# Kernel tuning notes

Measured on AMD Instinct MI355X. Metric: run time of the kernel, lower is better.

## Reference

```python
import jax, jax.numpy as jnp
import numpy as np

B, H, T, D = 2, 8, 2048, 64
STATE = H * D  # 512

def setup_inputs() -> dict:
    key = jax.random.key(0)
    kq, kk, kv, kw, kl = jax.random.split(key, 5)
    q = jax.random.normal(kq, (B * H, T, D), jnp.float32)
    k = jax.random.normal(kk, (B * H, T, D), jnp.float32)
    v = jax.random.normal(kv, (B * H, T, D), jnp.float32)
    # causal position mask: True = masked (future positions)
    position_mask = jnp.triu(jnp.ones((T, T), dtype=bool), 1)
    # per-batch source lengths in [T//2, T]; True = padding (masked)
    lengths = jax.random.randint(kl, (B,), T // 2, T + 1)
    src_length_mask = jnp.arange(T)[None, :] >= lengths[:, None]
    W_merge = jax.random.normal(kw, (STATE, STATE), jnp.float32) / np.sqrt(STATE)
    return {"q": q, "k": k, "v": v, "position_mask": position_mask,
            "src_length_mask": src_length_mask, "W_merge": W_merge}

def reference(q, k, v, position_mask, src_length_mask, W_merge):
    bb, n_dest, d = q.shape              # bb = B*H
    n_batch = src_length_mask.shape[0]
    n_heads = bb // n_batch
    scale = 1.0 / np.sqrt(d)
    # [bb, T_dest, T_src] full score matrix (as in the torch bmm)
    logits = jnp.einsum('btd,bsd->bts', q, k) * scale
    logits = logits.reshape(n_batch, n_heads, n_dest, -1)
    logits = jnp.where(position_mask[None, None], -jnp.inf, logits)
    logits = jnp.where(src_length_mask[:, None, None, :], -jnp.inf, logits)
    scores = jax.nn.softmax(logits, axis=-1).reshape(bb, n_dest, -1)
    # dropout p=0 (eval) -> identity
    out = jnp.einsum('bts,bsd->btd', scores, v)
    out = out.reshape(n_batch, n_heads, n_dest, d).transpose(0, 2, 1, 3)
    out = out.reshape(n_batch, n_dest, n_heads * d)
    return out @ W_merge.T  # bias-free Linear merge
```

## Files before the change

kernel.cpp:

```cpp
#include <hip/hip_runtime.h>

#define TT 2048
#define DD 64
#define NSTATE 512

typedef __attribute__((ext_vector_type(8))) short short8;
typedef __attribute__((ext_vector_type(4))) short short4v;
typedef __attribute__((ext_vector_type(4))) float f4;

__device__ __forceinline__ short f2bf(float x) {
  union { float f; unsigned u; } c; c.f = x;
  unsigned r = (c.u + 0x7FFFu + ((c.u >> 16) & 1u)) >> 16;
  return (short)r;
}

__device__ __forceinline__ bool mask_at(const void* p, bool u8, int idx) {
  return u8 ? (((const unsigned char*)p)[idx] != 0)
            : (((const int*)p)[idx] != 0);
}

__device__ __forceinline__ void gld16(const void* g, void* l) {
  __builtin_amdgcn_global_load_lds(
      (const __attribute__((address_space(1))) void*)g,
      (__attribute__((address_space(3))) void*)l, 16, 0, 0);
}

__global__ __launch_bounds__(256)
void prep_kernel(const float* __restrict__ k, const float* __restrict__ v,
                 const float* __restrict__ W, const void* __restrict__ posmask,
                 const void* __restrict__ srcmask,
                 unsigned short* __restrict__ Wb, unsigned short* __restrict__ Kimg,
                 unsigned short* __restrict__ VTimg, int* __restrict__ lenbuf) {
  const int bidx = blockIdx.x;
  const int tid = threadIdx.x;
  if (bidx < 512) {
    const int bh = bidx >> 5, tile = bidx & 31;
    const float* kp = k + (bh * TT + tile * 64) * DD;
    unsigned short* dst = Kimg + (bh * 32 + tile) * 4096;
#pragma unroll
    for (int t2 = 0; t2 < 2; ++t2) {
      int j = tid + t2 * 256;
      int c8 = j >> 6, r6 = j & 63;
      int kb = c8 >> 1, cc = c8 & 1, qd = r6 >> 4, klo = r6 & 15;
      int key = kb * 16 + klo, dg = cc * 4 + qd;
      f4 a0 = *(const f4*)(kp + key * DD + dg * 8);
      f4 a1 = *(const f4*)(kp + key * DD + dg * 8 + 4);
      short8 o;
      o[0]=f2bf(a0[0]); o[1]=f2bf(a0[1]); o[2]=f2bf(a0[2]); o[3]=f2bf(a0[3]);
      o[4]=f2bf(a1[0]); o[5]=f2bf(a1[1]); o[6]=f2bf(a1[2]); o[7]=f2bf(a1[3]);
      *(short8*)(dst + j * 8) = o;
    }
    __shared__ float Vt[64][65];
    const float* vp = v + (bh * TT + tile * 64) * DD;
    {
      int key = tid >> 2, c0 = (tid & 3) * 16;
#pragma unroll
      for (int i = 0; i < 4; ++i) {
        f4 x = *(const f4*)(vp + key * DD + c0 + i * 4);
        Vt[key][c0 + i * 4 + 0] = x[0];
        Vt[key][c0 + i * 4 + 1] = x[1];
        Vt[key][c0 + i * 4 + 2] = x[2];
        Vt[key][c0 + i * 4 + 3] = x[3];
      }
    }
    __syncthreads();
    unsigned short* vd = VTimg + (bh * 32 + tile) * 4096;
#pragma unroll
    for (int t2 = 0; t2 < 2; ++t2) {
      int j = tid + t2 * 256;
      int fs = j >> 5;
      int db = fs >> 2, sb = fs & 3;
      int jj = j & 31;
      short8 o;
#pragma unroll
      for (int ii = 0; ii < 8; ++ii) {
        int l = jj * 2 + (ii >> 2), r = ii & 3;
        int s = sb * 16 + (l >> 4) * 4 + r;
        int d = db * 16 + (l & 15);
        o[ii] = f2bf(Vt[s][d]);
      }
      *(short8*)(vd + j * 8) = o;
    }
  } else if (bidx < 768) {
    int i = ((bidx - 512) * 256 + tid) * 4;
    f4 x = *(const f4*)(W + i);
    short4v o;
    o[0]=f2bf(x[0]); o[1]=f2bf(x[1]); o[2]=f2bf(x[2]); o[3]=f2bf(x[3]);
    *(short4v*)(Wb + i) = o;
  } else {
    const int wv = tid >> 6, lane = tid & 63;
    if (wv < 2) {
      const bool u8 = (((const unsigned char*)posmask)[1] != 0);
      int pos = 1024 + lane * 16;
      bool m1 = mask_at(srcmask, u8, wv * TT + pos);
      unsigned long long bal = __ballot(m1);
      int cur = bal ? (1024 + (__ffsll((unsigned long long)bal) - 1) * 16) : 2048;
      int prev = cur - 16;
      bool m2 = false;
      if (lane < 16) {
        int pos2 = prev + 1 + lane;
        m2 = (pos2 < TT) ? mask_at(srcmask, u8, wv * TT + pos2) : true;
      }
      unsigned long long bal2 = __ballot(m2);
      int len = prev + 1 + (__ffsll((unsigned long long)bal2) - 1);
      if (lane == 0) lenbuf[wv] = len;
    }
  }
}

__global__ __launch_bounds__(512, 4)
void attn_kernel(const float* __restrict__ q, const unsigned short* __restrict__ Kimg,
                 const unsigned short* __restrict__ VTimg,
                 const int* __restrict__ lenbuf, unsigned short* __restrict__ merged) {
  const int i = blockIdx.x;
  const int bh = ((i & 7) << 1) | ((i >> 3) & 1);
  const int tr = i >> 4;
  const int tile = (tr < 16) ? tr : 47 - tr;
  const int b = bh >> 3, h = bh & 7;
  const int tid = threadIdx.x;
  const int w = tid >> 6, lane = tid & 63;
  const int g = w >> 2, wl = w & 3;
  const int lane_lo = lane & 15, quad = lane >> 4;
  const int q0 = tile * 64 + wl * 16;
  const int len = lenbuf[b];
  const int n_st = min(tile + 1, (len + 63) >> 6);
  const int trips = (n_st + 1) >> 1;

  __shared__ __attribute__((aligned(16))) unsigned short Klds[2][2][4096];
  __shared__ __attribute__((aligned(16))) unsigned short Vlds[2][2][4096];

  short8 qf[2];
  {
    const float* qrow = q + ((bh * TT) + q0 + lane_lo) * DD;
#pragma unroll
    for (int c = 0; c < 2; ++c) {
      int d0 = c * 32 + quad * 8;
      f4 a0 = *(const f4*)(qrow + d0);
      f4 a1 = *(const f4*)(qrow + d0 + 4);
      short8 t;
      t[0]=f2bf(a0[0]*0.125f); t[1]=f2bf(a0[1]*0.125f);
      t[2]=f2bf(a0[2]*0.125f); t[3]=f2bf(a0[3]*0.125f);
      t[4]=f2bf(a1[0]*0.125f); t[5]=f2bf(a1[1]*0.125f);
      t[6]=f2bf(a1[2]*0.125f); t[7]=f2bf(a1[3]*0.125f);
      qf[c] = t;
    }
  }

  float l_lane = 0.f;
  f4 O[4];
#pragma unroll
  for (int d = 0; d < 4; ++d) O[d] = (f4){0.f, 0.f, 0.f, 0.f};

  const char* kbase = (const char*)Kimg + (size_t)bh * 262144;
  const char* vbase = (const char*)VTimg + (size_t)bh * 262144;

  auto stage = [&](int st, int bufi) {
    const char* ks = kbase + st * 8192 + wl * 2048 + lane * 16;
    char* kl = (char*)&Klds[g][bufi][0] + wl * 2048 + lane * 16;
    gld16(ks, kl); gld16(ks + 1024, kl + 1024);
    const char* vs = vbase + st * 8192 + wl * 2048 + lane * 16;
    char* vl = (char*)&Vlds[g][bufi][0] + wl * 2048 + lane * 16;
    gld16(vs, vl); gld16(vs + 1024, vl + 1024);
  };

  if (g < n_st) stage(g, 0);
  __syncthreads();

  for (int it = 0; it < trips; ++it) {
    const int st = 2 * it + g;
    const int bufc = it & 1;
    const int st_next = st + 2;
    if (st_next < n_st) stage(st_next, bufc ^ 1);
    if (st < n_st) {
      const unsigned short* Kl = &Klds[g][bufc][0];
      const unsigned short* Vl = &Vlds[g][bufc][0];
      const int s0 = st * 64;

      f4 ST[4];
      __builtin_amdgcn_s_setprio(1);
#pragma unroll
      for (int sb = 0; sb < 4; ++sb) {
        f4 acc = (f4){0.f, 0.f, 0.f, 0.f};
#pragma unroll
        for (int c = 0; c < 2; ++c) {
          short8 kf = *(const short8*)&Kl[((sb * 2 + c) * 64 + lane) * 8];
          acc = __builtin_amdgcn_mfma_f32_16x16x32_bf16(kf, qf[c], acc, 0, 0, 0);
        }
        ST[sb] = acc;
      }
      __builtin_amdgcn_s_setprio(0);

      const bool edge = (st == tile) || (s0 + 64 > len);
      const int tq = q0 + lane_lo;
      short4v pf[4];
#pragma unroll
      for (int sb = 0; sb < 4; ++sb)
#pragma unroll
        for (int r = 0; r < 4; ++r) {
          float p = __expf(ST[sb][r]);
          if (edge) {
            int s = s0 + sb * 16 + quad * 4 + r;
            if (s > tq || s >= len) p = 0.f;
          }
          l_lane += p;
          pf[sb][r] = f2bf(p);
        }

      __builtin_amdgcn_s_setprio(1);
#pragma unroll
      for (int db = 0; db < 4; ++db) {
        f4 acc = O[db];
#pragma unroll
        for (int sb = 0; sb < 4; ++sb) {
          short4v vf = *(const short4v*)&Vl[(db * 4 + sb) * 256 + lane * 4];
          acc = __builtin_amdgcn_mfma_f32_16x16x16bf16_1k(pf[sb], vf, acc, 0, 0, 0);
        }
        O[db] = acc;
      }
      __builtin_amdgcn_s_setprio(0);
    }
    __syncthreads();
  }

  l_lane += __shfl_xor(l_lane, 16);
  l_lane += __shfl_xor(l_lane, 32);

  float* Ored = (float*)&Klds[1][0][0];
  float* lred = (float*)&Vlds[1][0][0];
  if (g == 1) {
    float* po = Ored + (wl * 64 + lane) * 16;
#pragma unroll
    for (int db = 0; db < 4; ++db) *(f4*)(po + db * 4) = O[db];
    lred[wl * 64 + lane] = l_lane;
  }
  __syncthreads();
  if (g == 0) {
    const float* po = Ored + (wl * 64 + lane) * 16;
#pragma unroll
    for (int db = 0; db < 4; ++db) {
      f4 o1 = *(const f4*)(po + db * 4);
      O[db][0] += o1[0]; O[db][1] += o1[1];
      O[db][2] += o1[2]; O[db][3] += o1[3];
    }
    l_lane += lred[wl * 64 + lane];
    float inv = 1.0f / l_lane;
    float invr[4];
#pragma unroll
    for (int r = 0; r < 4; ++r) invr[r] = __shfl(inv, quad * 4 + r);
#pragma unroll
    for (int db = 0; db < 4; ++db)
#pragma unroll
      for (int r = 0; r < 4; ++r) {
        int t = q0 + quad * 4 + r;
        merged[((b * TT) + t) * NSTATE + h * DD + db * 16 + lane_lo] =
            (unsigned short)f2bf(O[db][r] * invr[r]);
      }
  }
}

__global__ __launch_bounds__(512)
void merge_kernel(const unsigned short* __restrict__ A,
                  const unsigned short* __restrict__ Wb,
                  float* __restrict__ out) {
  __shared__ __attribute__((aligned(16))) unsigned short Wl[64 * 512];
  const int tid = threadIdx.x;
  const int n0 = blockIdx.x * 64, m0 = blockIdx.y * 128;
  {
    int row = tid >> 3, cb = (tid & 7) * 8;
    const unsigned short* src = Wb + (n0 + row) * NSTATE;
#pragma unroll
    for (int j = 0; j < 8; ++j) {
      int c = cb + j;
      int phys = c ^ (row & 7);
      *(short8*)&Wl[row * 512 + phys * 8] = *(const short8*)(src + c * 8);
    }
  }
  __syncthreads();

  const int w = tid >> 6, lane = tid & 63;
  const int lo16 = lane & 15, quad = lane >> 4;
  const int m = m0 + w * 16;
  f4 acc[4];
#pragma unroll
  for (int nf = 0; nf < 4; ++nf) acc[nf] = (f4){0.f, 0.f, 0.f, 0.f};
  const unsigned short* arow = A + (m + lo16) * NSTATE + quad * 8;
#pragma unroll 4
  for (int k0 = 0; k0 < NSTATE; k0 += 32) {
    short8 af = *(const short8*)(arow + k0);
#pragma unroll
    for (int nf = 0; nf < 4; ++nf) {
      int n = nf * 16 + lo16;
      int phys = ((k0 >> 3) + quad) ^ (n & 7);
      short8 bf = *(const short8*)&Wl[n * 512 + phys * 8];
      acc[nf] = __builtin_amdgcn_mfma_f32_16x16x32_bf16(af, bf, acc[nf], 0, 0, 0);
    }
  }
#pragma unroll
  for (int nf = 0; nf < 4; ++nf)
#pragma unroll
    for (int r = 0; r < 4; ++r)
      out[(m + quad * 4 + r) * NSTATE + n0 + nf * 16 + lo16] = acc[nf][r];
}

extern "C" void kernel_launch(void* const* d_in, const int* in_sizes, int n_in,
                              void* d_out, int out_size, void* d_ws, size_t ws_size,
                              hipStream_t stream) {
  (void)in_sizes; (void)n_in; (void)out_size; (void)ws_size;
  const float* q = (const float*)d_in[0];
  const float* k = (const float*)d_in[1];
  const float* v = (const float*)d_in[2];
  const void* posm = d_in[3];
  const void* srcm = d_in[4];
  const float* W = (const float*)d_in[5];
  float* out = (float*)d_out;

  unsigned short* merged = (unsigned short*)d_ws;
  unsigned short* Wb     = merged + 2097152;
  unsigned short* Kimg   = Wb + 262144;
  unsigned short* VTimg  = Kimg + 2097152;
  int* lenbuf = (int*)(VTimg + 2097152);

  prep_kernel<<<dim3(769), dim3(256), 0, stream>>>(k, v, W, posm, srcm,
                                                   Wb, Kimg, VTimg, lenbuf);
  attn_kernel<<<dim3(512), dim3(512), 0, stream>>>(q, Kimg, VTimg, lenbuf, merged);
  merge_kernel<<<dim3(8, 32), dim3(512), 0, stream>>>(merged, Wb, out);
}
```

Measured before the change: 122.2 us.

## Use hardware bf16 pack conversion and partial vmcnt waits in attention loop

Replaces the software round-to-nearest bf16 conversion with the packed v_cvt_pk_bf16_f32 instruction across the prep, attention and output paths. In the attention loop, the full __syncthreads is swapped for explicit s_waitcnt vmcnt(4)/vmcnt(0) plus a raw s_barrier with sched_barrier fences. Only the current stage's async LDS loads are waited on, so the prefetch of the next stage stays in flight. This cuts conversion ALU work and lets loads overlap compute, but relies on hand-counted outstanding-load numbers and compiler scheduling fences, so a miscount would silently read stale data.

```diff
diff --git a/kernel.cpp b/kernel.cpp
--- a/kernel.cpp
+++ b/kernel.cpp
@@ -8,10 +8,16 @@
 typedef __attribute__((ext_vector_type(4))) short short4v;
 typedef __attribute__((ext_vector_type(4))) float f4;
 
-__device__ __forceinline__ short f2bf(float x) {
-  union { float f; unsigned u; } c; c.f = x;
-  unsigned r = (c.u + 0x7FFFu + ((c.u >> 16) & 1u)) >> 16;
-  return (short)r;
+union U8 { short8 s; unsigned u[4]; };
+union U4 { short4v s; unsigned u[2]; };
+
+__device__ __forceinline__ unsigned pk_bf16(float lo, float hi) {
+  unsigned r;
+  asm("v_cvt_pk_bf16_f32 %0, %1, %2" : "=v"(r) : "v"(lo), "v"(hi));
+  return r;
+}
+__device__ __forceinline__ unsigned short f2bf1(float x) {
+  return (unsigned short)(pk_bf16(x, x) & 0xFFFFu);
 }
 
 __device__ __forceinline__ bool mask_at(const void* p, bool u8, int idx) {
@@ -45,10 +51,10 @@
       int key = kb * 16 + klo, dg = cc * 4 + qd;
       f4 a0 = *(const f4*)(kp + key * DD + dg * 8);
       f4 a1 = *(const f4*)(kp + key * DD + dg * 8 + 4);
-      short8 o;
-      o[0]=f2bf(a0[0]); o[1]=f2bf(a0[1]); o[2]=f2bf(a0[2]); o[3]=f2bf(a0[3]);
-      o[4]=f2bf(a1[0]); o[5]=f2bf(a1[1]); o[6]=f2bf(a1[2]); o[7]=f2bf(a1[3]);
-      *(short8*)(dst + j * 8) = o;
+      U8 o;
+      o.u[0] = pk_bf16(a0[0], a0[1]); o.u[1] = pk_bf16(a0[2], a0[3]);
+      o.u[2] = pk_bf16(a1[0], a1[1]); o.u[3] = pk_bf16(a1[2], a1[3]);
+      *(short8*)(dst + j * 8) = o.s;
     }
     __shared__ float Vt[64][65];
     const float* vp = v + (bh * TT + tile * 64) * DD;
@@ -71,22 +77,25 @@
       int fs = j >> 5;
       int db = fs >> 2, sb = fs & 3;
       int jj = j & 31;
-      short8 o;
+      float t[8];
 #pragma unroll
       for (int ii = 0; ii < 8; ++ii) {
         int l = jj * 2 + (ii >> 2), r = ii & 3;
         int s = sb * 16 + (l >> 4) * 4 + r;
         int d = db * 16 + (l & 15);
-        o[ii] = f2bf(Vt[s][d]);
-      }
-      *(short8*)(vd + j * 8) = o;
+        t[ii] = Vt[s][d];
+      }
+      U8 o;
+      o.u[0] = pk_bf16(t[0], t[1]); o.u[1] = pk_bf16(t[2], t[3]);
+      o.u[2] = pk_bf16(t[4], t[5]); o.u[3] = pk_bf16(t[6], t[7]);
+      *(short8*)(vd + j * 8) = o.s;
     }
   } else if (bidx < 768) {
     int i = ((bidx - 512) * 256 + tid) * 4;
     f4 x = *(const f4*)(W + i);
-    short4v o;
-    o[0]=f2bf(x[0]); o[1]=f2bf(x[1]); o[2]=f2bf(x[2]); o[3]=f2bf(x[3]);
-    *(short4v*)(Wb + i) = o;
+    U4 o;
+    o.u[0] = pk_bf16(x[0], x[1]); o.u[1] = pk_bf16(x[2], x[3]);
+    *(short4v*)(Wb + i) = o.s;
   } else {
     const int wv = tid >> 6, lane = tid & 63;
     if (wv < 2) {
@@ -137,14 +146,15 @@
       int d0 = c * 32 + quad * 8;
       f4 a0 = *(const f4*)(qrow + d0);
       f4 a1 = *(const f4*)(qrow + d0 + 4);
-      short8 t;
-      t[0]=f2bf(a0[0]*0.125f); t[1]=f2bf(a0[1]*0.125f);
-      t[2]=f2bf(a0[2]*0.125f); t[3]=f2bf(a0[3]*0.125f);
-      t[4]=f2bf(a1[0]*0.125f); t[5]=f2bf(a1[1]*0.125f);
-      t[6]=f2bf(a1[2]*0.125f); t[7]=f2bf(a1[3]*0.125f);
-      qf[c] = t;
-    }
-  }
+      U8 t;
+      t.u[0] = pk_bf16(a0[0] * 0.125f, a0[1] * 0.125f);
+      t.u[1] = pk_bf16(a0[2] * 0.125f, a0[3] * 0.125f);
+      t.u[2] = pk_bf16(a1[0] * 0.125f, a1[1] * 0.125f);
+      t.u[3] = pk_bf16(a1[2] * 0.125f, a1[3] * 0.125f);
+      qf[c] = t.s;
+    }
+  }
+  asm volatile("s_waitcnt vmcnt(0)" ::: "memory");
 
   float l_lane = 0.f;
   f4 O[4];
@@ -164,13 +174,19 @@
   };
 
   if (g < n_st) stage(g, 0);
-  __syncthreads();
 
   for (int it = 0; it < trips; ++it) {
     const int st = 2 * it + g;
     const int bufc = it & 1;
-    const int st_next = st + 2;
-    if (st_next < n_st) stage(st_next, bufc ^ 1);
+    if (st + 2 < n_st) {
+      stage(st + 2, bufc ^ 1);
+      asm volatile("s_waitcnt vmcnt(4)" ::: "memory");
+    } else {
+      asm volatile("s_waitcnt vmcnt(0)" ::: "memory");
+    }
+    __builtin_amdgcn_s_barrier();
+    __builtin_amdgcn_sched_barrier(0);
+
     if (st < n_st) {
       const unsigned short* Kl = &Klds[g][bufc][0];
       const unsigned short* Vl = &Vlds[g][bufc][0];
@@ -194,7 +210,8 @@
       const int tq = q0 + lane_lo;
       short4v pf[4];
 #pragma unroll
-      for (int sb = 0; sb < 4; ++sb)
+      for (int sb = 0; sb < 4; ++sb) {
+        float e[4];
 #pragma unroll
         for (int r = 0; r < 4; ++r) {
           float p = __expf(ST[sb][r]);
@@ -203,8 +220,13 @@
             if (s > tq || s >= len) p = 0.f;
           }
           l_lane += p;
-          pf[sb][r] = f2bf(p);
+          e[r] = p;
         }
+        U4 pu;
+        pu.u[0] = pk_bf16(e[0], e[1]);
+        pu.u[1] = pk_bf16(e[2], e[3]);
+        pf[sb] = pu.s;
+      }
 
       __builtin_amdgcn_s_setprio(1);
 #pragma unroll
@@ -219,7 +241,8 @@
       }
       __builtin_amdgcn_s_setprio(0);
     }
-    __syncthreads();
+    __builtin_amdgcn_sched_barrier(0);
+    __builtin_amdgcn_s_barrier();
   }
 
   l_lane += __shfl_xor(l_lane, 16);
@@ -253,7 +276,7 @@
       for (int r = 0; r < 4; ++r) {
         int t = q0 + quad * 4 + r;
         merged[((b * TT) + t) * NSTATE + h * DD + db * 16 + lane_lo] =
-            (unsigned short)f2bf(O[db][r] * invr[r]);
+            f2bf1(O[db][r] * invr[r]);
       }
   }
 }
```

Measured after the change: 121.1 us. About the same (-1.0%).
